# Kernel optimization log

Hardware: AMD Instinct MI355X
Metric: run time of the kernel (lower is better)

The kernel has to match this reference:

```python
import jax, jax.numpy as jnp
import numpy as np

TOL_A = 1e-09


def setup_inputs() -> dict:
    key = jax.random.key(0)
    ks = jax.random.split(key, 6)
    nx, nu, ny, bsz, T = 256, 128, 128, 128, 2048
    return {
        "u": jax.random.normal(ks[0], (bsz, T, nu), jnp.float32),
        "M": jax.random.normal(ks[1], (2 * nx, 2 * nx), jnp.float32),
        "B": jax.random.normal(ks[2], (nx, nu), jnp.float32),
        "C": jax.random.normal(ks[3], (ny, nx), jnp.float32),
        "D": jax.random.normal(ks[4], (ny, nu), jnp.float32),
        "x0": jax.random.normal(ks[5], (nx, 1), jnp.float32),
    }


def _compute_A(M):
    # LMI-based stable A: S = M M^T + tol*I; A = E^{-1} F
    nx = M.shape[0] // 2
    S = M @ M.T + TOL_A * jnp.eye(2 * nx, dtype=M.dtype)
    F = S[nx:, :nx]
    P = S[nx:, nx:]
    E = 0.5 * (P + S[:nx, :nx])
    return jnp.linalg.solve(E, F)  # == inv(E) @ F


def reference(u, M, B, C, D, x0):
    # u: (bsz, T, nu); returns predictions (bsz, T, ny)
    nx = B.shape[0]
    A = _compute_A(M)  # time-invariant: computed once instead of per step
    bsz = u.shape[0]
    x = jnp.broadcast_to(x0[:, 0], (bsz, nx))  # learned x0 stacked over batch
    # t=0 output: C x0 + D u_0 (faithful to torch code)
    y0 = x @ C.T + u[:, 0] @ D.T

    def step(x, u_t):
        # x_{t+1} = A x_t + B u_t ; y_{t+1} = C x_{t+1} + D u_t (off-by-one D term, as in source)
        x = x @ A.T + u_t @ B.T
        y = x @ C.T + u_t @ D.T
        return x, y

    # scan over time: xs is (T-1, bsz, nu)
    _, ys = jax.lax.scan(step, x, jnp.swapaxes(u[:, :-1], 0, 1))
    preds = jnp.concatenate([y0[None], ys], axis=0)  # (T, bsz, ny)
    return jnp.swapaxes(preds, 0, 1)
```

## Files before the change

### kernel.cpp

```cpp
#include <hip/hip_runtime.h>

#define NX 256
#define NU 128
#define NY 128
#define BSZ 128
#define TT 2048
#define LCH 32
#define KCH 64

typedef _Float16 h8 __attribute__((ext_vector_type(8)));
typedef _Float16 h4 __attribute__((ext_vector_type(4)));
typedef float f4 __attribute__((ext_vector_type(4)));

__device__ __forceinline__ f4 mfma16(h8 a, h8 b, f4 c) {
  return __builtin_amdgcn_mfma_f32_16x16x32_f16(a, b, c, 0, 0, 0);
}
#define PIN(x) asm volatile("" : "+v"(x))
#define LBAR() asm volatile("s_waitcnt lgkmcnt(0)\n\ts_barrier" ::: "memory")

__device__ __forceinline__ int swz256(int row, int bc) { return row * 256 + (bc ^ ((row & 7) << 4)); }
__device__ __forceinline__ int xwSwz(int row, int canon) {
  return row * 512 + (canon ^ ((row & 7) << 4) ^ ((canon & 16) << 1));
}

__device__ __forceinline__ h8 cvt8(f4 lo, f4 hi) {
  h8 h;
#pragma unroll
  for (int j = 0; j < 4; ++j) { h[j] = (_Float16)lo[j]; h[j + 4] = (_Float16)hi[j]; }
  return h;
}
__device__ __forceinline__ h4 h4cvt(f4 v) {
  h4 h;
#pragma unroll
  for (int j = 0; j < 4; ++j) h[j] = (_Float16)v[j];
  return h;
}
__device__ __forceinline__ h8 h8zero() {
  h8 h;
#pragma unroll
  for (int j = 0; j < 8; ++j) h[j] = (_Float16)0.0f;
  return h;
}

__device__ __forceinline__ void mm_core(const float* __restrict__ a, const float* __restrict__ b,
                                        int Nb, int i0, int j0, int tid,
                                        float (*As)[32][65], float (*Bs)[64][33],
                                        float acc[2][2]) {
  const int ar = tid >> 4, ac = (tid & 15) * 4;
  const int br = tid >> 3, bc = (tid & 7) * 4;
  const int tx = tid & 15, ty = tid >> 4;
  f4 pa0 = *(const f4*)(a + (size_t)(i0 + ar) * 256 + ac);
  f4 pa1 = *(const f4*)(a + (size_t)(i0 + ar + 16) * 256 + ac);
  f4 pb0 = *(const f4*)(b + (size_t)br * Nb + j0 + bc);
  f4 pb1 = *(const f4*)(b + (size_t)(br + 32) * Nb + j0 + bc);
  for (int r4 = 0; r4 < 4; ++r4) {
    const int bs = r4 & 1;
#pragma unroll
    for (int m = 0; m < 4; ++m) {
      As[bs][ar][ac + m] = pa0[m];
      As[bs][ar + 16][ac + m] = pa1[m];
      Bs[bs][br][bc + m] = pb0[m];
      Bs[bs][br + 32][bc + m] = pb1[m];
    }
    if (r4 < 3) {
      int kk = (r4 + 1) * 64;
      pa0 = *(const f4*)(a + (size_t)(i0 + ar) * 256 + kk + ac);
      pa1 = *(const f4*)(a + (size_t)(i0 + ar + 16) * 256 + kk + ac);
      pb0 = *(const f4*)(b + (size_t)(kk + br) * Nb + j0 + bc);
      pb1 = *(const f4*)(b + (size_t)(kk + br + 32) * Nb + j0 + bc);
    }
    __syncthreads();
#pragma unroll 8
    for (int k = 0; k < 64; ++k) {
      float a0 = As[bs][ty * 2][k], a1 = As[bs][ty * 2 + 1][k];
      float b0 = Bs[bs][k][tx * 2], b1 = Bs[bs][k][tx * 2 + 1];
      acc[0][0] += a0 * b0; acc[0][1] += a0 * b1;
      acc[1][0] += a1 * b0; acc[1][1] += a1 * b1;
    }
  }
}

__global__ __launch_bounds__(256) void k_ef(const float* __restrict__ M, const float* __restrict__ B,
                                            const float* __restrict__ C, const float* __restrict__ D,
                                            const float* __restrict__ x0, const float* __restrict__ u,
                                            float* __restrict__ E, float* __restrict__ F,
                                            _Float16* __restrict__ B16, float* __restrict__ out) {
  const int tid = threadIdx.x;
  int z = blockIdx.x >> 6;
  if (z >= 2) {
    if (blockIdx.x < 192) {
      int idx = (blockIdx.x - 128) * 256 + tid;
      int b = idx >> 7, col = idx & 127;
      const float* crow = C + (size_t)col * 256;
      const float* drow = D + (size_t)col * 128;
      const float* ur = u + (size_t)b * (TT * NU);
      float s = 0.f;
#pragma unroll 8
      for (int j = 0; j < 256; j += 4) {
        f4 cv = *(const f4*)(crow + j);
        f4 xv = *(const f4*)(x0 + j);
        s += cv[0] * xv[0] + cv[1] * xv[1] + cv[2] * xv[2] + cv[3] * xv[3];
      }
#pragma unroll 8
      for (int j = 0; j < 128; j += 4) {
        f4 dv = *(const f4*)(drow + j);
        f4 uv = *(const f4*)(ur + j);
        s += dv[0] * uv[0] + dv[1] * uv[1] + dv[2] * uv[2] + dv[3] * uv[3];
      }
      out[(size_t)b * (TT * NY) + col] = s;
    } else {
      int i = (blockIdx.x - 192) * 1024 + tid;
      B16[i] = (_Float16)B[i];
      B16[i + 256] = (_Float16)B[i + 256];
      B16[i + 512] = (_Float16)B[i + 512];
      B16[i + 768] = (_Float16)B[i + 768];
    }
    return;
  }
  __shared__ float Ps[2][32][65], Qs[2][32][65];
  int tile = blockIdx.x & 63;
  int i0 = (tile >> 3) * 32, j0 = (tile & 7) * 32;
  const int ar = tid >> 4, ac = (tid & 15) * 4;
  const int tx = tid & 15, ty = tid >> 4;
  float acc[2][2] = {{0.f, 0.f}, {0.f, 0.f}};
  int np = (z == 0) ? 2 : 1;
  int rc = 0;
  for (int p = 0; p < np; ++p) {
    int po = (z == 0) ? p * 256 : 256;
    int qo = (z == 0) ? p * 256 : 0;
    f4 p0 = *(const f4*)(M + (size_t)(i0 + po + ar) * 512 + ac);
    f4 p1 = *(const f4*)(M + (size_t)(i0 + po + ar + 16) * 512 + ac);
    f4 q0 = *(const f4*)(M + (size_t)(j0 + qo + ar) * 512 + ac);
    f4 q1 = *(const f4*)(M + (size_t)(j0 + qo + ar + 16) * 512 + ac);
    for (int kk = 0; kk < 512; kk += 64) {
      const int bs = rc & 1;
      ++rc;
#pragma unroll
      for (int m = 0; m < 4; ++m) {
        Ps[bs][ar][ac + m] = p0[m];
        Ps[bs][ar + 16][ac + m] = p1[m];
        Qs[bs][ar][ac + m] = q0[m];
        Qs[bs][ar + 16][ac + m] = q1[m];
      }
      if (kk < 448) {
        int k2 = kk + 64;
        p0 = *(const f4*)(M + (size_t)(i0 + po + ar) * 512 + k2 + ac);
        p1 = *(const f4*)(M + (size_t)(i0 + po + ar + 16) * 512 + k2 + ac);
        q0 = *(const f4*)(M + (size_t)(j0 + qo + ar) * 512 + k2 + ac);
        q1 = *(const f4*)(M + (size_t)(j0 + qo + ar + 16) * 512 + k2 + ac);
      }
      __syncthreads();
#pragma unroll 8
      for (int k = 0; k < 64; ++k) {
        float a0 = Ps[bs][ty * 2][k], a1 = Ps[bs][ty * 2 + 1][k];
        float b0 = Qs[bs][tx * 2][k], b1 = Qs[bs][tx * 2 + 1][k];
        acc[0][0] += a0 * b0; acc[0][1] += a0 * b1;
        acc[1][0] += a1 * b0; acc[1][1] += a1 * b1;
      }
    }
  }
#pragma unroll
  for (int ii = 0; ii < 2; ++ii)
#pragma unroll
    for (int jj = 0; jj < 2; ++jj) {
      int i = i0 + ty * 2 + ii, j = j0 + tx * 2 + jj;
      if (z == 0) {
        float v = 0.5f * acc[ii][jj];
        if (i == j) v += 1e-9f;
        E[i * 256 + j] = v;
      } else {
        F[i * 256 + j] = acc[ii][jj];
      }
    }
}

__global__ __launch_bounds__(256) void k_ns0(const float* __restrict__ E,
                                             float* __restrict__ X, float* __restrict__ Y) {
  __shared__ float As[2][32][65];
  __shared__ float Bs[2][64][33];
  __shared__ float s1[256], red[256];
  const int tid = threadIdx.x;
  {
    float s = 0.f;
    const float* row = E + (size_t)tid * 256;
#pragma unroll 8
    for (int j = 0; j < 256; j += 4) {
      f4 e = *(const f4*)(row + j);
      s += e[0] + e[1] + e[2] + e[3];
    }
    s1[tid] = s; red[tid] = s * s;
  }
  __syncthreads();
  for (int o = 128; o > 0; o >>= 1) { if (tid < o) red[tid] += red[tid + o]; __syncthreads(); }
  float n1 = red[0];
  __syncthreads();
  {
    float s = 0.f;
    const float* row = E + (size_t)tid * 256;
#pragma unroll 8
    for (int j = 0; j < 256; j += 4) {
      f4 e = *(const f4*)(row + j);
      f4 vv = *(const f4*)(&s1[j]);
      s += e[0] * vv[0] + e[1] * vv[1] + e[2] * vv[2] + e[3] * vv[3];
    }
    red[tid] = s * s;
  }
  __syncthreads();
  for (int o = 128; o > 0; o >>= 1) { if (tid < o) red[tid] += red[tid + o]; __syncthreads(); }
  float c = sqrtf(n1 / red[0]);
  __syncthreads();
  if (blockIdx.x < 64) {
    int i0 = (blockIdx.x >> 3) * 32, j0 = (blockIdx.x & 7) * 32;
    float acc[2][2] = {{0.f, 0.f}, {0.f, 0.f}};
    mm_core(E, E, 256, i0, j0, tid, As, Bs, acc);
    int tx = tid & 15, ty = tid >> 4;
#pragma unroll
    for (int ii = 0; ii < 2; ++ii)
#pragma unroll
      for (int jj = 0; jj < 2; ++jj) {
        int i = i0 + ty * 2 + ii, j = j0 + tx * 2 + jj;
        Y[(size_t)i * 256 + j] = 2.f * c * E[(size_t)i * 256 + j] - c * c * acc[ii][jj];
      }
  } else {
    int idx = (blockIdx.x - 64) * 1024 + tid * 4;
    int i = idx >> 8, j = idx & 255;
    f4 e = *(const f4*)(E + idx);
    f4 v;
#pragma unroll
    for (int m = 0; m < 4; ++m) v[m] = ((j + m) == i ? 2.f * c : 0.f) - c * c * e[m];
    *(f4*)(X + idx) = v;
  }
}

struct MMJob {
  const float* a; const float* b; const float* add;
  float* d32; _Float16* d16;
  int M, N, mode, blk0;
};

__global__ __launch_bounds__(256) void k_mm(MMJob j0, MMJob j1, MMJob j2, int njobs) {
  __shared__ float As[2][32][65];
  __shared__ float Bs[2][64][33];
  const int tid = threadIdx.x;
  int bid = blockIdx.x;
  MMJob jb = j0;
  if (njobs > 1 && bid >= j1.blk0) jb = j1;
  if (njobs > 2 && bid >= j2.blk0) jb = j2;
  int rel = bid - jb.blk0;
  int ntile = jb.N >> 5;
  int i0 = (rel / ntile) * 32, j0g = (rel % ntile) * 32;
  float acc[2][2] = {{0.f, 0.f}, {0.f, 0.f}};
  mm_core(jb.a, jb.b, jb.N, i0, j0g, tid, As, Bs, acc);
  int tx = tid & 15, ty = tid >> 4;
#pragma unroll
  for (int ii = 0; ii < 2; ++ii)
#pragma unroll
    for (int jj = 0; jj < 2; ++jj) {
      int i = i0 + ty * 2 + ii, j = j0g + tx * 2 + jj;
      size_t o = (size_t)i * jb.N + j;
      float v = acc[ii][jj];
      if (jb.mode == 1) v = 2.f * jb.a[(size_t)i * 256 + j] - v;
      else if (jb.add) v += jb.add[o];
      if (jb.d32) jb.d32[o] = v;
      if (jb.d16) jb.d16[o] = (_Float16)v;
    }
}

__global__ __launch_bounds__(512, 2) void k_recW(const float* __restrict__ u,
                                                 const _Float16* __restrict__ A16,
                                                 const _Float16* __restrict__ B16,
                                                 float* __restrict__ w) {
  __shared__ __align__(16) char sm[24576];
  char* xb = sm;
  char* ub = sm + 16384;
  const int tid = threadIdx.x, lane = tid & 63, wv = tid >> 6;
  const int g = lane >> 4, lr = lane & 15;
  const int chunk = blockIdx.x >> 3, btile = blockIdx.x & 7;
  const int b0 = btile * 16, t0 = chunk * LCH, nt0 = wv * 2;

  h8 Ar[2][8], Bf[2][4];
#pragma unroll
  for (int n2 = 0; n2 < 2; ++n2) {
#pragma unroll
    for (int kf = 0; kf < 8; ++kf) {
      Ar[n2][kf] = *(const h8*)(A16 + (size_t)((nt0 + n2) * 16 + lr) * NX + kf * 32 + g * 8);
      PIN(Ar[n2][kf]);
    }
#pragma unroll
    for (int kf = 0; kf < 4; ++kf) {
      Bf[n2][kf] = *(const h8*)(B16 + (size_t)((nt0 + n2) * 16 + lr) * NU + kf * 32 + g * 8);
      PIN(Bf[n2][kf]);
    }
  }
  const int urow = tid >> 5, uuc = tid & 31;
  const float* ubase = u + (size_t)(b0 + urow) * (TT * NU) + uuc * 4;
  const int uoff = swz256(urow, uuc * 8);
  {
    f4 r0 = *(const f4*)(ubase + (size_t)t0 * NU);
    *(h4*)(ub + uoff) = h4cvt(r0);
  }
  f4 urA = *(const f4*)(ubase + (size_t)(t0 + 1) * NU);
  f4 urB = *(const f4*)(ubase + (size_t)(t0 + 2 < TT ? t0 + 2 : TT - 1) * NU);
  h8 af[8];
#pragma unroll
  for (int kf = 0; kf < 8; ++kf) af[kf] = h8zero();
  __syncthreads();

  f4 z4 = {0.f, 0.f, 0.f, 0.f};
  f4 xacc[2];
#pragma unroll 2
  for (int i = 0; i < LCH; ++i) {
    const int p = i & 1;
    if (i < LCH - 1) {
      int nt = t0 + i + 3;
      if (nt > TT - 1) nt = TT - 1;
      if (p == 0) {
        *(h4*)(ub + 4096 + uoff) = h4cvt(urA);
        urA = *(const f4*)(ubase + (size_t)nt * NU);
      } else {
        *(h4*)(ub + uoff) = h4cvt(urB);
        urB = *(const f4*)(ubase + (size_t)nt * NU);
      }
    }
    h8 uf[4];
#pragma unroll
    for (int kf = 0; kf < 4; ++kf)
      uf[kf] = *(const h8*)(ub + p * 4096 + swz256(lr, kf * 64 + g * 16));
    __builtin_amdgcn_s_setprio(1);
    xacc[0] = z4; xacc[1] = z4;
#pragma unroll
    for (int kf = 0; kf < 8; ++kf) {
      xacc[0] = mfma16(Ar[0][kf], af[kf], xacc[0]);
      xacc[1] = mfma16(Ar[1][kf], af[kf], xacc[1]);
    }
#pragma unroll
    for (int kf = 0; kf < 4; ++kf) {
      xacc[0] = mfma16(Bf[0][kf], uf[kf], xacc[0]);
      xacc[1] = mfma16(Bf[1][kf], uf[kf], xacc[1]);
    }
    __builtin_amdgcn_s_setprio(0);
    if (i < LCH - 1) {
#pragma unroll
      for (int n2 = 0; n2 < 2; ++n2)
        *(h4*)(xb + (p ^ 1) * 8192 + xwSwz(lr, (nt0 + n2) * 32 + g * 8)) = h4cvt(xacc[n2]);
      LBAR();
#pragma unroll
      for (int kf = 0; kf < 8; ++kf)
        af[kf] = *(const h8*)(xb + (p ^ 1) * 8192 + xwSwz(lr, kf * 64 + g * 16));
    }
  }
#pragma unroll
  for (int n2 = 0; n2 < 2; ++n2)
    *(f4*)(w + ((size_t)chunk * BSZ + b0 + lr) * NX + (nt0 + n2) * 16 + g * 4) = xacc[n2];
}

__global__ __launch_bounds__(512, 2) void k_phB(const float* __restrict__ x0,
                                                const float* __restrict__ w,
                                                const _Float16* __restrict__ Ah16,
                                                float* __restrict__ xs) {
  __shared__ __align__(16) char xb[16384];
  const int tid = threadIdx.x, lane = tid & 63, wv = tid >> 6;
  const int g = lane >> 4, lr = lane & 15;
  const int b0 = blockIdx.x * 16, nt0 = wv * 2;
  h8 Ar[2][8];
#pragma unroll
  for (int n2 = 0; n2 < 2; ++n2)
#pragma unroll
    for (int kf = 0; kf < 8; ++kf) {
      Ar[n2][kf] = *(const h8*)(Ah16 + (size_t)((nt0 + n2) * 16 + lr) * NX + kf * 32 + g * 8);
      PIN(Ar[n2][kf]);
    }
  for (int s = 0; s < 8; ++s) {
    int e = tid + s * 512;
    int row = e >> 8, c = e & 255;
    xs[(size_t)(b0 + row) * NX + c] = x0[c];
  }
  h8 af[8];
#pragma unroll
  for (int kf = 0; kf < 8; ++kf) {
    const float* sp = x0 + kf * 32 + g * 8;
    af[kf] = cvt8(*(const f4*)sp, *(const f4*)(sp + 4));
  }
  f4 wl[2];
#pragma unroll
  for (int n2 = 0; n2 < 2; ++n2)
    wl[n2] = *(const f4*)(w + ((size_t)0 * BSZ + b0 + lr) * NX + (nt0 + n2) * 16 + g * 4);
  f4 z4 = {0.f, 0.f, 0.f, 0.f};
  for (int k = 0; k < KCH - 1; ++k) {
    const int p = k & 1;
    f4 wn[2] = {z4, z4};
    if (k < KCH - 2) {
#pragma unroll
      for (int n2 = 0; n2 < 2; ++n2)
        wn[n2] = *(const f4*)(w + ((size_t)(k + 1) * BSZ + b0 + lr) * NX + (nt0 + n2) * 16 + g * 4);
    }
    f4 acc[2] = {z4, z4};
#pragma unroll
    for (int kf = 0; kf < 8; ++kf) {
      acc[0] = mfma16(Ar[0][kf], af[kf], acc[0]);
      acc[1] = mfma16(Ar[1][kf], af[kf], acc[1]);
    }
#pragma unroll
    for (int n2 = 0; n2 < 2; ++n2) {
      acc[n2] += wl[n2];
      *(f4*)(xs + ((size_t)(k + 1) * BSZ + b0 + lr) * NX + (nt0 + n2) * 16 + g * 4) = acc[n2];
    }
    if (k < KCH - 2) {
#pragma unroll
      for (int n2 = 0; n2 < 2; ++n2)
        *(h4*)(xb + (p ^ 1) * 8192 + xwSwz(lr, (nt0 + n2) * 32 + g * 8)) = h4cvt(acc[n2]);
      LBAR();
#pragma unroll
      for (int kf = 0; kf < 8; ++kf)
        af[kf] = *(const h8*)(xb + (p ^ 1) * 8192 + xwSwz(lr, kf * 64 + g * 16));
    }
#pragma unroll
    for (int n2 = 0; n2 < 2; ++n2) wl[n2] = wn[n2];
  }
}

__global__ __launch_bounds__(512, 2) void k_recY(const float* __restrict__ u,
                                                 const _Float16* __restrict__ A16,
                                                 const _Float16* __restrict__ B16,
                                                 const _Float16* __restrict__ CA16,
                                                 const _Float16* __restrict__ CBD16,
                                                 const float* __restrict__ xs,
                                                 float* __restrict__ out) {
  __shared__ __align__(16) char sm[24576];
  char* xb = sm;
  char* ub = sm + 16384;
  const int tid = threadIdx.x, lane = tid & 63, wv = tid >> 6;
  const int g = lane >> 4, lr = lane & 15;
  const int chunk = blockIdx.x >> 3, btile = blockIdx.x & 7;
  const int b0 = btile * 16, t0 = chunk * LCH, nt0 = wv * 2;

  h8 Ar[2][8], Bf[2][4], Cf[8], Df[4];
#pragma unroll
  for (int n2 = 0; n2 < 2; ++n2) {
#pragma unroll
    for (int kf = 0; kf < 8; ++kf) {
      Ar[n2][kf] = *(const h8*)(A16 + (size_t)((nt0 + n2) * 16 + lr) * NX + kf * 32 + g * 8);
      PIN(Ar[n2][kf]);
    }
#pragma unroll
    for (int kf = 0; kf < 4; ++kf) {
      Bf[n2][kf] = *(const h8*)(B16 + (size_t)((nt0 + n2) * 16 + lr) * NU + kf * 32 + g * 8);
      PIN(Bf[n2][kf]);
    }
  }
#pragma unroll
  for (int kf = 0; kf < 8; ++kf) {
    Cf[kf] = *(const h8*)(CA16 + (size_t)(wv * 16 + lr) * NX + kf * 32 + g * 8);
    PIN(Cf[kf]);
  }
#pragma unroll
  for (int kf = 0; kf < 4; ++kf) {
    Df[kf] = *(const h8*)(CBD16 + (size_t)(wv * 16 + lr) * NU + kf * 32 + g * 8);
    PIN(Df[kf]);
  }
  h8 af[8];
#pragma unroll
  for (int kf = 0; kf < 8; ++kf) {
    const float* sp = xs + ((size_t)chunk * BSZ + b0 + lr) * NX + kf * 32 + g * 8;
    af[kf] = cvt8(*(const f4*)sp, *(const f4*)(sp + 4));
  }
  const int urow = tid >> 5, uuc = tid & 31;
  const float* ubase = u + (size_t)(b0 + urow) * (TT * NU) + uuc * 4;
  const int uoff = swz256(urow, uuc * 8);
  float* obase = out + (size_t)(b0 + lr) * (TT * NY) + wv * 16 + g * 4;
  {
    f4 r0 = *(const f4*)(ubase + (size_t)t0 * NU);
    *(h4*)(ub + uoff) = h4cvt(r0);
  }
  f4 urA = *(const f4*)(ubase + (size_t)(t0 + 1) * NU);
  f4 urB = *(const f4*)(ubase + (size_t)(t0 + 2 < TT ? t0 + 2 : TT - 1) * NU);
  __syncthreads();

  f4 z4 = {0.f, 0.f, 0.f, 0.f};
#pragma unroll 2
  for (int i = 0; i < LCH; ++i) {
    const int p = i & 1;
    if (i < LCH - 1) {
      int nt = t0 + i + 3;
      if (nt > TT - 1) nt = TT - 1;
      if (p == 0) {
        *(h4*)(ub + 4096 + uoff) = h4cvt(urA);
        urA = *(const f4*)(ubase + (size_t)nt * NU);
      } else {
        *(h4*)(ub + uoff) = h4cvt(urB);
        urB = *(const f4*)(ubase + (size_t)nt * NU);
      }
    }
    h8 uf[4];
#pragma unroll
    for (int kf = 0; kf < 4; ++kf)
      uf[kf] = *(const h8*)(ub + p * 4096 + swz256(lr, kf * 64 + g * 16));
    if (i < LCH - 1) {
      __builtin_amdgcn_s_setprio(1);
      f4 xacc[2] = {z4, z4};
#pragma unroll
      for (int kf = 0; kf < 8; ++kf) {
        xacc[0] = mfma16(Ar[0][kf], af[kf], xacc[0]);
        xacc[1] = mfma16(Ar[1][kf], af[kf], xacc[1]);
      }
#pragma unroll
      for (int kf = 0; kf < 4; ++kf) {
        xacc[0] = mfma16(Bf[0][kf], uf[kf], xacc[0]);
        xacc[1] = mfma16(Bf[1][kf], uf[kf], xacc[1]);
      }
      __builtin_amdgcn_s_setprio(0);
#pragma unroll
      for (int n2 = 0; n2 < 2; ++n2)
        *(h4*)(xb + (p ^ 1) * 8192 + xwSwz(lr, (nt0 + n2) * 32 + g * 8)) = h4cvt(xacc[n2]);
    }
    __builtin_amdgcn_s_setprio(1);
    f4 yacc = z4;
#pragma unroll
    for (int kf = 0; kf < 8; ++kf) yacc = mfma16(Cf[kf], af[kf], yacc);
#pragma unroll
    for (int kf = 0; kf < 4; ++kf) yacc = mfma16(Df[kf], uf[kf], yacc);
    __builtin_amdgcn_s_setprio(0);
    int t = t0 + i + 1;
    if (t < TT) *(f4*)(obase + (size_t)t * NY) = yacc;
    if (i < LCH - 1) {
      LBAR();
#pragma unroll
      for (int kf = 0; kf < 8; ++kf)
        af[kf] = *(const h8*)(xb + (p ^ 1) * 8192 + xwSwz(lr, kf * 64 + g * 16));
    }
  }
}

extern "C" void kernel_launch(void* const* d_in, const int* in_sizes, int n_in,
                              void* d_out, int out_size, void* d_ws, size_t ws_size,
                              hipStream_t stream) {
  const float* u  = (const float*)d_in[0];
  const float* M  = (const float*)d_in[1];
  const float* B  = (const float*)d_in[2];
  const float* C  = (const float*)d_in[3];
  const float* D  = (const float*)d_in[4];
  const float* x0 = (const float*)d_in[5];
  float* out = (float*)d_out;
  char* ws = (char*)d_ws;

  float* E    = (float*)(ws + 0L);
  float* F    = (float*)(ws + 256L * 1024);
  float* X1   = (float*)(ws + 512L * 1024);
  float* Y1   = (float*)(ws + 768L * 1024);
  float* X2   = (float*)(ws + 1024L * 1024);
  float* Y2   = (float*)(ws + 1280L * 1024);
  float* Amat = (float*)(ws + 1536L * 1024);
  float* P2   = (float*)(ws + 1792L * 1024);
  float* P4   = (float*)(ws + 2048L * 1024);
  float* P8   = (float*)(ws + 2304L * 1024);
  float* P16  = (float*)(ws + 2560L * 1024);
  _Float16* A16   = (_Float16*)(ws + 2816L * 1024);
  _Float16* Ah16  = (_Float16*)(ws + 2944L * 1024);
  _Float16* B16   = (_Float16*)(ws + 3072L * 1024);
  _Float16* CA16  = (_Float16*)(ws + 3136L * 1024);
  _Float16* CBD16 = (_Float16*)(ws + 3200L * 1024);
  float* wbuf = (float*)(ws + 9408L * 1024);
  float* xs   = (float*)(ws + 17600L * 1024);

  MMJob nil = {nullptr, nullptr, nullptr, nullptr, nullptr, 0, 0, 0, 0};

  k_ef<<<224, 256, 0, stream>>>(M, B, C, D, x0, u, E, F, B16, out);
  k_ns0<<<128, 256, 0, stream>>>(E, X1, Y1);
  float *Xc = X1, *Yc = Y1, *Xn = X2, *Yn = Y2;
  for (int it = 0; it < 6; ++it) {
    MMJob jx = {Xc, Yc, nullptr, Xn, nullptr, 256, 256, 1, 0};
    MMJob jy = {Yc, Yc, nullptr, Yn, nullptr, 256, 256, 1, 64};
    k_mm<<<128, 256, 0, stream>>>(jx, jy, nil, 2);
    float* t1 = Xc; Xc = Xn; Xn = t1;
    float* t2 = Yc; Yc = Yn; Yn = t2;
  }
  {
    MMJob ja = {Xc, F, nullptr, Amat, A16, 256, 256, 0, 0};
    k_mm<<<64, 256, 0, stream>>>(ja, nil, nil, 1);
  }
  {
    MMJob j0 = {Amat, Amat, nullptr, P2, nullptr, 256, 256, 0, 0};
    MMJob j1 = {C, Amat, nullptr, nullptr, CA16, 128, 256, 0, 64};
    MMJob j2 = {C, B, D, nullptr, CBD16, 128, 128, 0, 96};
    k_mm<<<112, 256, 0, stream>>>(j0, j1, j2, 3);
  }
  {
    MMJob j0 = {P2, P2, nullptr, P4, nullptr, 256, 256, 0, 0};
    k_mm<<<64, 256, 0, stream>>>(j0, nil, nil, 1);
  }
  {
    MMJob j0 = {P4, P4, nullptr, P8, nullptr, 256, 256, 0, 0};
    k_mm<<<64, 256, 0, stream>>>(j0, nil, nil, 1);
  }
  {
    MMJob j0 = {P8, P8, nullptr, P16, nullptr, 256, 256, 0, 0};
    k_mm<<<64, 256, 0, stream>>>(j0, nil, nil, 1);
  }
  {
    MMJob j0 = {P16, P16, nullptr, nullptr, Ah16, 256, 256, 0, 0};
    k_mm<<<64, 256, 0, stream>>>(j0, nil, nil, 1);
  }

  k_recW<<<512, 512, 0, stream>>>(u, A16, B16, wbuf);
  k_phB<<<8, 512, 0, stream>>>(x0, wbuf, Ah16, xs);
  k_recY<<<512, 512, 0, stream>>>(u, A16, B16, CA16, CBD16, xs, out);
}
```

Baseline: 347.5 us.

## Advance chunk recurrence two steps per iteration using A^2 and AB

The per-chunk state recurrence in k_recW now advances two timesteps per iteration, x_{t+2} = A^2 x_t + AB u_t + B u_{t+1}. This halves the number of serial barrier-separated steps from 32 to 16. A^2 and A·B are precomputed in half precision by extending existing matmul launches, and the u staging buffer grows to four slots. Each iteration does more MFMA work (16 extra instructions) and the larger LDS footprint may reduce occupancy. Using an fp16 A^2 may also change the numerical error.

```diff
diff --git a/kernel.cpp b/kernel.cpp
--- a/kernel.cpp
+++ b/kernel.cpp
@@ -267,10 +267,11 @@
 }
 
 __global__ __launch_bounds__(512, 2) void k_recW(const float* __restrict__ u,
-                                                 const _Float16* __restrict__ A16,
+                                                 const _Float16* __restrict__ A216,
+                                                 const _Float16* __restrict__ AB16,
                                                  const _Float16* __restrict__ B16,
                                                  float* __restrict__ w) {
-  __shared__ __align__(16) char sm[24576];
+  __shared__ __align__(16) char sm[32768];
   char* xb = sm;
   char* ub = sm + 16384;
   const int tid = threadIdx.x, lane = tid & 63, wv = tid >> 6;
@@ -278,16 +279,18 @@
   const int chunk = blockIdx.x >> 3, btile = blockIdx.x & 7;
   const int b0 = btile * 16, t0 = chunk * LCH, nt0 = wv * 2;
 
-  h8 Ar[2][8], Bf[2][4];
+  h8 A2f[2][8], ABf[2][4], Bf[2][4];
 #pragma unroll
   for (int n2 = 0; n2 < 2; ++n2) {
 #pragma unroll
     for (int kf = 0; kf < 8; ++kf) {
-      Ar[n2][kf] = *(const h8*)(A16 + (size_t)((nt0 + n2) * 16 + lr) * NX + kf * 32 + g * 8);
-      PIN(Ar[n2][kf]);
+      A2f[n2][kf] = *(const h8*)(A216 + (size_t)((nt0 + n2) * 16 + lr) * NX + kf * 32 + g * 8);
+      PIN(A2f[n2][kf]);
     }
 #pragma unroll
     for (int kf = 0; kf < 4; ++kf) {
+      ABf[n2][kf] = *(const h8*)(AB16 + (size_t)((nt0 + n2) * 16 + lr) * NU + kf * 32 + g * 8);
+      PIN(ABf[n2][kf]);
       Bf[n2][kf] = *(const h8*)(B16 + (size_t)((nt0 + n2) * 16 + lr) * NU + kf * 32 + g * 8);
       PIN(Bf[n2][kf]);
     }
@@ -298,9 +301,11 @@
   {
     f4 r0 = *(const f4*)(ubase + (size_t)t0 * NU);
     *(h4*)(ub + uoff) = h4cvt(r0);
-  }
-  f4 urA = *(const f4*)(ubase + (size_t)(t0 + 1) * NU);
-  f4 urB = *(const f4*)(ubase + (size_t)(t0 + 2 < TT ? t0 + 2 : TT - 1) * NU);
+    f4 r1 = *(const f4*)(ubase + (size_t)(t0 + 1) * NU);
+    *(h4*)(ub + 4096 + uoff) = h4cvt(r1);
+  }
+  f4 urA = *(const f4*)(ubase + (size_t)(t0 + 2) * NU);
+  f4 urB = *(const f4*)(ubase + (size_t)(t0 + 3) * NU);
   h8 af[8];
 #pragma unroll
   for (int kf = 0; kf < 8; ++kf) af[kf] = h8zero();
@@ -309,44 +314,50 @@
   f4 z4 = {0.f, 0.f, 0.f, 0.f};
   f4 xacc[2];
 #pragma unroll 2
-  for (int i = 0; i < LCH; ++i) {
-    const int p = i & 1;
-    if (i < LCH - 1) {
-      int nt = t0 + i + 3;
-      if (nt > TT - 1) nt = TT - 1;
-      if (p == 0) {
-        *(h4*)(ub + 4096 + uoff) = h4cvt(urA);
-        urA = *(const f4*)(ubase + (size_t)nt * NU);
-      } else {
-        *(h4*)(ub + uoff) = h4cvt(urB);
-        urB = *(const f4*)(ubase + (size_t)nt * NU);
-      }
-    }
-    h8 uf[4];
-#pragma unroll
-    for (int kf = 0; kf < 4; ++kf)
-      uf[kf] = *(const h8*)(ub + p * 4096 + swz256(lr, kf * 64 + g * 16));
+  for (int p = 0; p < 16; ++p) {
+    const int q = p & 1;
+    const int s0 = (2 * p) & 3, s1 = (2 * p + 1) & 3;
+    if (p < 15) {
+      *(h4*)(ub + ((2 * p + 2) & 3) * 4096 + uoff) = h4cvt(urA);
+      *(h4*)(ub + ((2 * p + 3) & 3) * 4096 + uoff) = h4cvt(urB);
+      int na = t0 + 2 * p + 4, nb = t0 + 2 * p + 5;
+      if (na > TT - 1) na = TT - 1;
+      if (nb > TT - 1) nb = TT - 1;
+      urA = *(const f4*)(ubase + (size_t)na * NU);
+      urB = *(const f4*)(ubase + (size_t)nb * NU);
+    }
+    h8 ufa[4], ufb[4];
+#pragma unroll
+    for (int kf = 0; kf < 4; ++kf) {
+      ufa[kf] = *(const h8*)(ub + s0 * 4096 + swz256(lr, kf * 64 + g * 16));
+      ufb[kf] = *(const h8*)(ub + s1 * 4096 + swz256(lr, kf * 64 + g * 16));
+    }
     __builtin_amdgcn_s_setprio(1);
     xacc[0] = z4; xacc[1] = z4;
 #pragma unroll
     for (int kf = 0; kf < 8; ++kf) {
-      xacc[0] = mfma16(Ar[0][kf], af[kf], xacc[0]);
-      xacc[1] = mfma16(Ar[1][kf], af[kf], xacc[1]);
+      xacc[0] = mfma16(A2f[0][kf], af[kf], xacc[0]);
+      xacc[1] = mfma16(A2f[1][kf], af[kf], xacc[1]);
     }
 #pragma unroll
     for (int kf = 0; kf < 4; ++kf) {
-      xacc[0] = mfma16(Bf[0][kf], uf[kf], xacc[0]);
-      xacc[1] = mfma16(Bf[1][kf], uf[kf], xacc[1]);
+      xacc[0] = mfma16(ABf[0][kf], ufa[kf], xacc[0]);
+      xacc[1] = mfma16(ABf[1][kf], ufa[kf], xacc[1]);
+    }
+#pragma unroll
+    for (int kf = 0; kf < 4; ++kf) {
+      xacc[0] = mfma16(Bf[0][kf], ufb[kf], xacc[0]);
+      xacc[1] = mfma16(Bf[1][kf], ufb[kf], xacc[1]);
     }
     __builtin_amdgcn_s_setprio(0);
-    if (i < LCH - 1) {
+    if (p < 15) {
 #pragma unroll
       for (int n2 = 0; n2 < 2; ++n2)
-        *(h4*)(xb + (p ^ 1) * 8192 + xwSwz(lr, (nt0 + n2) * 32 + g * 8)) = h4cvt(xacc[n2]);
+        *(h4*)(xb + (q ^ 1) * 8192 + xwSwz(lr, (nt0 + n2) * 32 + g * 8)) = h4cvt(xacc[n2]);
       LBAR();
 #pragma unroll
       for (int kf = 0; kf < 8; ++kf)
-        af[kf] = *(const h8*)(xb + (p ^ 1) * 8192 + xwSwz(lr, kf * 64 + g * 16));
+        af[kf] = *(const h8*)(xb + (q ^ 1) * 8192 + xwSwz(lr, kf * 64 + g * 16));
     }
   }
 #pragma unroll
@@ -559,6 +570,8 @@
   _Float16* B16   = (_Float16*)(ws + 3072L * 1024);
   _Float16* CA16  = (_Float16*)(ws + 3136L * 1024);
   _Float16* CBD16 = (_Float16*)(ws + 3200L * 1024);
+  _Float16* A216  = (_Float16*)(ws + 3264L * 1024);
+  _Float16* AB16  = (_Float16*)(ws + 3392L * 1024);
   float* wbuf = (float*)(ws + 9408L * 1024);
   float* xs   = (float*)(ws + 17600L * 1024);
 
@@ -579,14 +592,15 @@
     k_mm<<<64, 256, 0, stream>>>(ja, nil, nil, 1);
   }
   {
-    MMJob j0 = {Amat, Amat, nullptr, P2, nullptr, 256, 256, 0, 0};
+    MMJob j0 = {Amat, Amat, nullptr, P2, A216, 256, 256, 0, 0};
     MMJob j1 = {C, Amat, nullptr, nullptr, CA16, 128, 256, 0, 64};
     MMJob j2 = {C, B, D, nullptr, CBD16, 128, 128, 0, 96};
     k_mm<<<112, 256, 0, stream>>>(j0, j1, j2, 3);
   }
   {
     MMJob j0 = {P2, P2, nullptr, P4, nullptr, 256, 256, 0, 0};
-    k_mm<<<64, 256, 0, stream>>>(j0, nil, nil, 1);
+    MMJob j1 = {Amat, B, nullptr, nullptr, AB16, 256, 128, 0, 64};
+    k_mm<<<96, 256, 0, stream>>>(j0, j1, nil, 2);
   }
   {
     MMJob j0 = {P4, P4, nullptr, P8, nullptr, 256, 256, 0, 0};
@@ -601,7 +615,7 @@
     k_mm<<<64, 256, 0, stream>>>(j0, nil, nil, 1);
   }
 
-  k_recW<<<512, 512, 0, stream>>>(u, A16, B16, wbuf);
+  k_recW<<<512, 512, 0, stream>>>(u, A216, AB16, B16, wbuf);
   k_phB<<<8, 512, 0, stream>>>(x0, wbuf, Ah16, xs);
   k_recY<<<512, 512, 0, stream>>>(u, A16, B16, CA16, CBD16, xs, out);
 }
```

After: 339.6 us (median of 2 runs). 1.02x faster.
